# Optimization experiments

Measured on AMD Instinct MI355X. Metric: run time of the kernel, lower is better.

The kernel has to match this reference:

```python
import jax, jax.numpy as jnp
import numpy as np

N_AGENTS = 8
STATE_DIM = 256
EMBED_DIM = 32
BATCH = 65536


def setup_inputs() -> dict:
    key = jax.random.key(0)
    ks = jax.random.split(key, 12)
    s = 1.0 / np.sqrt(STATE_DIM)
    se = 1.0 / np.sqrt(EMBED_DIM)
    return {
        "agent_qs": jax.random.normal(ks[0], (BATCH, N_AGENTS), dtype=jnp.float32),
        "states": jax.random.normal(ks[1], (BATCH, STATE_DIM), dtype=jnp.float32),
        # hyper_w_1: Linear(state_dim, embed_dim * n_agents)
        "w1_W": jax.random.uniform(ks[2], (STATE_DIM, EMBED_DIM * N_AGENTS), jnp.float32, -s, s),
        "w1_b": jax.random.uniform(ks[3], (EMBED_DIM * N_AGENTS,), jnp.float32, -s, s),
        # hyper_w_final: Linear(state_dim, embed_dim)
        "wf_W": jax.random.uniform(ks[4], (STATE_DIM, EMBED_DIM), jnp.float32, -s, s),
        "wf_b": jax.random.uniform(ks[5], (EMBED_DIM,), jnp.float32, -s, s),
        # hyper_b_1: Linear(state_dim, embed_dim)
        "b1_W": jax.random.uniform(ks[6], (STATE_DIM, EMBED_DIM), jnp.float32, -s, s),
        "b1_b": jax.random.uniform(ks[7], (EMBED_DIM,), jnp.float32, -s, s),
        # V: Linear(state_dim, embed_dim) -> ReLU -> Linear(embed_dim, 1)
        "v1_W": jax.random.uniform(ks[8], (STATE_DIM, EMBED_DIM), jnp.float32, -s, s),
        "v1_b": jax.random.uniform(ks[9], (EMBED_DIM,), jnp.float32, -s, s),
        "v2_W": jax.random.uniform(ks[10], (EMBED_DIM, 1), jnp.float32, -se, se),
        "v2_b": jax.random.uniform(ks[11], (1,), jnp.float32, -se, se),
    }


def reference(agent_qs, states, w1_W, w1_b, wf_W, wf_b, b1_W, b1_b, v1_W, v1_b, v2_W, v2_b):
    B = agent_qs.shape[0]
    # hypernet weights (abs for monotonicity)
    w1 = jnp.abs(states @ w1_W + w1_b).reshape(B, N_AGENTS, EMBED_DIM)   # [B, A, E]
    w_final = jnp.abs(states @ wf_W + wf_b)                               # [B, E]
    b1 = states @ b1_W + b1_b                                             # [B, E]
    # hidden = elu(agent_qs^T w1 + b1): [B,1,A] @ [B,A,E] -> [B,E]
    hidden = jax.nn.elu(jnp.einsum("ba,bae->be", agent_qs, w1) + b1)
    # mixed = hidden @ w_final: [B,1,E] @ [B,E,1] -> [B,1]
    mixed = jnp.sum(hidden * w_final, axis=-1, keepdims=True)             # [B, 1]
    # state value V(s)
    state_value = jax.nn.relu(states @ v1_W + v1_b) @ v2_W + v2_b         # [B, 1]
    return mixed + state_value
```

## Files before the change

kernel.cpp:

```cpp
#include <hip/hip_runtime.h>
#include <math.h>


#define NTILES 22
#define KCHUNKS 8
#define CHUNK_I4 1408

typedef __attribute__((ext_vector_type(8))) short short8;
typedef __attribute__((ext_vector_type(4))) float float4v;

__device__ __forceinline__ unsigned short f2b(float f) {
    unsigned int u = __float_as_uint(f);
    u = u + 0x7fffu + ((u >> 16) & 1u);
    return (unsigned short)(u >> 16);
}

__device__ __forceinline__ void gl2lds16(const unsigned short* g, unsigned short* l) {
    __builtin_amdgcn_global_load_lds(
        (const __attribute__((address_space(1))) unsigned int*)g,
        (__attribute__((address_space(3))) unsigned int*)l,
        16, 0, 0);
}

__global__ void repack_b(const float* __restrict__ w1_W,
                         const float* __restrict__ wf_W,
                         const float* __restrict__ b1_W,
                         const float* __restrict__ v1_W,
                         unsigned short* __restrict__ brep) {
    int idx = blockIdx.x * 256 + threadIdx.x;
    int lane = idx & 63;
    int tt   = idx >> 6;
    int t    = tt % 22;
    int kc   = tt / 22;
    int kbase = kc * 32 + (lane >> 4) * 8;
    int n = t * 16 + (lane & 15);
    short8 frag;
#pragma unroll
    for (int j = 0; j < 8; ++j) {
        int k = kbase + j;
        float val;
        if (n < 256)      val = w1_W[k * 256 + n];
        else if (n < 288) val = wf_W[k * 32 + (n - 256)];
        else if (n < 320) val = b1_W[k * 32 + (n - 288)];
        else              val = v1_W[k * 32 + (n - 320)];
        frag[j] = (short)f2b(val);
    }
    *(short8*)(&brep[idx * 8]) = frag;
}

__global__ void __launch_bounds__(256, 2)
qmix_main(const float* __restrict__ agent_qs,
          const float* __restrict__ states,
          const unsigned short* __restrict__ brep,
          const float* __restrict__ w1_b,
          const float* __restrict__ wf_b,
          const float* __restrict__ b1_b,
          const float* __restrict__ v1_b,
          const float* __restrict__ v2_W,
          const float* __restrict__ v2_b,
          float* __restrict__ out) {
    __shared__ __align__(16) unsigned short wlds[2][NTILES * 64 * 8];

    const int tid  = threadIdx.x;
    const int wave = tid >> 6, lane = tid & 63;
    const int quad = lane >> 4, l16 = lane & 15;
    const int r0 = blockIdx.x * 128 + wave * 32 + l16;
    const float* srow0 = states + (size_t)r0 * 256;
    const float* srow1 = srow0 + 16 * 256;

    for (int s = wave; s < NTILES; s += 4)
        gl2lds16(brep + (size_t)(s * 64 + lane) * 8, wlds[0] + s * 512);

    float4v s0a = *(const float4v*)(srow0 + quad * 8);
    float4v s0b = *(const float4v*)(srow0 + quad * 8 + 4);
    float4v s1a = *(const float4v*)(srow1 + quad * 8);
    float4v s1b = *(const float4v*)(srow1 + quad * 8 + 4);

    float4v acc[2][NTILES];
#pragma unroll
    for (int g = 0; g < 2; ++g)
#pragma unroll
        for (int t = 0; t < NTILES; ++t)
#pragma unroll
            for (int q = 0; q < 4; ++q) acc[g][t][q] = 0.f;

    __syncthreads();

    int cur = 0;
    for (int kc = 0; kc < KCHUNKS; ++kc) {
        if (kc < KCHUNKS - 1) {
            const unsigned short* src = brep + (size_t)(kc + 1) * CHUNK_I4 * 8;
            unsigned short* dst = wlds[cur ^ 1];
            for (int s = wave; s < NTILES; s += 4)
                gl2lds16(src + (size_t)(s * 64 + lane) * 8, dst + s * 512);
        }
        short8 b0, b1;
#pragma unroll
        for (int j = 0; j < 4; ++j) {
            b0[j] = (short)f2b(s0a[j]); b0[4 + j] = (short)f2b(s0b[j]);
            b1[j] = (short)f2b(s1a[j]); b1[4 + j] = (short)f2b(s1b[j]);
        }
        if (kc < KCHUNKS - 1) {
            const float* p0 = srow0 + (kc + 1) * 32 + quad * 8;
            const float* p1 = srow1 + (kc + 1) * 32 + quad * 8;
            s0a = *(const float4v*)(p0);
            s0b = *(const float4v*)(p0 + 4);
            s1a = *(const float4v*)(p1);
            s1b = *(const float4v*)(p1 + 4);
        }
        const short8* wb = (const short8*)wlds[cur] + lane;
#pragma unroll
        for (int t = 0; t < NTILES; ++t) {
            short8 af = wb[t * 64];
            acc[0][t] = __builtin_amdgcn_mfma_f32_16x16x32_bf16(af, b0, acc[0][t], 0, 0, 0);
            acc[1][t] = __builtin_amdgcn_mfma_f32_16x16x32_bf16(af, b1, acc[1][t], 0, 0, 0);
        }
        cur ^= 1;
        __syncthreads();
    }

#pragma unroll
    for (int g = 0; g < 2; ++g) {
        const int row = r0 + g * 16;
        float4v q0 = *(const float4v*)(agent_qs + (size_t)row * 8);
        float4v q1 = *(const float4v*)(agent_qs + (size_t)row * 8 + 4);
        float qv[8] = {q0[0], q0[1], q0[2], q0[3], q1[0], q1[1], q1[2], q1[3]};

        float qacc[8], wfv[8], b1v[8], svp = 0.f;
#pragma unroll
        for (int s = 0; s < 8; ++s) qacc[s] = 0.f;

#pragma unroll
        for (int t = 0; t < NTILES; ++t) {
            const float* bptr =
                (t < 16) ? (w1_b + t * 16) :
                (t < 18) ? (wf_b + (t - 16) * 16) :
                (t < 20) ? (b1_b + (t - 18) * 16) : (v1_b + (t - 20) * 16);
            float4v bb = *(const float4v*)(bptr + quad * 4);
            float vb[4];
#pragma unroll
            for (int j = 0; j < 4; ++j) vb[j] = acc[g][t][j] + bb[j];

            if (t < 16) {
                float q = qv[t >> 1];
                int base = (t & 1) * 4;
#pragma unroll
                for (int j = 0; j < 4; ++j) qacc[base + j] += q * fabsf(vb[j]);
            } else if (t < 18) {
                int base = (t - 16) * 4;
#pragma unroll
                for (int j = 0; j < 4; ++j) wfv[base + j] = fabsf(vb[j]);
            } else if (t < 20) {
                int base = (t - 18) * 4;
#pragma unroll
                for (int j = 0; j < 4; ++j) b1v[base + j] = vb[j];
            } else {
                int ebase = (t - 20) * 16 + quad * 4;
#pragma unroll
                for (int j = 0; j < 4; ++j)
                    svp += fmaxf(vb[j], 0.f) * v2_W[ebase + j];
            }
        }

        float mix = 0.f;
#pragma unroll
        for (int s = 0; s < 8; ++s) {
            float h = qacc[s] + b1v[s];
            h = h > 0.f ? h : (__expf(h) - 1.f);
            mix += h * wfv[s];
        }
        float tot = mix + svp;
        tot += __shfl_xor(tot, 16);
        tot += __shfl_xor(tot, 32);
        if (quad == 0) out[row] = tot + v2_b[0];
    }
}

extern "C" void kernel_launch(void* const* d_in, const int* in_sizes, int n_in,
                              void* d_out, int out_size, void* d_ws, size_t ws_size,
                              hipStream_t stream) {
    const float* agent_qs = (const float*)d_in[0];
    const float* states   = (const float*)d_in[1];
    const float* w1_W = (const float*)d_in[2];
    const float* w1_b = (const float*)d_in[3];
    const float* wf_W = (const float*)d_in[4];
    const float* wf_b = (const float*)d_in[5];
    const float* b1_W = (const float*)d_in[6];
    const float* b1_b = (const float*)d_in[7];
    const float* v1_W = (const float*)d_in[8];
    const float* v1_b = (const float*)d_in[9];
    const float* v2_W = (const float*)d_in[10];
    const float* v2_b = (const float*)d_in[11];
    float* out = (float*)d_out;
    unsigned short* brep = (unsigned short*)d_ws;

    repack_b<<<44, 256, 0, stream>>>(w1_W, wf_W, b1_W, v1_W, brep);
    qmix_main<<<512, 256, 0, stream>>>(agent_qs, states, brep,
                                       w1_b, wf_b, b1_b, v1_b, v2_W, v2_b, out);
}
```

Before: 127.0 us.

## Keep w1 weights resident in LDS, stream small tiles from global, double block size

The repacked weights are reordered so all 16 w1 tiles across every K chunk (128 slots, 128 KB) are loaded into LDS once at kernel start. The remaining 6 tiles (wf, b1, v1) are read per chunk straight from global/L2 into registers. This removes the per-chunk double-buffered LDS refill and the __syncthreads in the K loop. Blocks grow to 512 threads covering 256 rows each, with half as many blocks. The 128 KB LDS footprint limits occupancy to at most one block per CU, even though launch bounds ask for two, and the direct global loads of the small tiles sit on the MFMA critical path.

```diff
diff --git a/kernel.cpp b/kernel.cpp
--- a/kernel.cpp
+++ b/kernel.cpp
@@ -4,7 +4,7 @@
 
 #define NTILES 22
 #define KCHUNKS 8
-#define CHUNK_I4 1408
+#define LDS_SLOTS 128
 
 typedef __attribute__((ext_vector_type(8))) short short8;
 typedef __attribute__((ext_vector_type(4))) float float4v;
@@ -29,9 +29,10 @@
                          unsigned short* __restrict__ brep) {
     int idx = blockIdx.x * 256 + threadIdx.x;
     int lane = idx & 63;
-    int tt   = idx >> 6;
-    int t    = tt % 22;
-    int kc   = tt / 22;
+    int slot = idx >> 6;
+    int t, kc;
+    if (slot < 128) { t = slot >> 3; kc = slot & 7; }
+    else            { int r = slot - 128; kc = r / 6; t = 16 + r % 6; }
     int kbase = kc * 32 + (lane >> 4) * 8;
     int n = t * 16 + (lane & 15);
     short8 frag;
@@ -48,7 +49,7 @@
     *(short8*)(&brep[idx * 8]) = frag;
 }
 
-__global__ void __launch_bounds__(256, 2)
+__global__ void __launch_bounds__(512, 2)
 qmix_main(const float* __restrict__ agent_qs,
           const float* __restrict__ states,
           const unsigned short* __restrict__ brep,
@@ -59,17 +60,17 @@
           const float* __restrict__ v2_W,
           const float* __restrict__ v2_b,
           float* __restrict__ out) {
-    __shared__ __align__(16) unsigned short wlds[2][NTILES * 64 * 8];
+    __shared__ __align__(16) unsigned short wlds[LDS_SLOTS * 64 * 8];
 
     const int tid  = threadIdx.x;
     const int wave = tid >> 6, lane = tid & 63;
     const int quad = lane >> 4, l16 = lane & 15;
-    const int r0 = blockIdx.x * 128 + wave * 32 + l16;
+    const int r0 = blockIdx.x * 256 + wave * 32 + l16;
     const float* srow0 = states + (size_t)r0 * 256;
     const float* srow1 = srow0 + 16 * 256;
 
-    for (int s = wave; s < NTILES; s += 4)
-        gl2lds16(brep + (size_t)(s * 64 + lane) * 8, wlds[0] + s * 512);
+    for (int s = wave; s < LDS_SLOTS; s += 8)
+        gl2lds16(brep + (size_t)(s * 64 + lane) * 8, wlds + s * 512);
 
     float4v s0a = *(const float4v*)(srow0 + quad * 8);
     float4v s0b = *(const float4v*)(srow0 + quad * 8 + 4);
@@ -86,14 +87,13 @@
 
     __syncthreads();
 
-    int cur = 0;
+    const short8* wl = (const short8*)wlds + lane;
+    const short8* ws = (const short8*)brep + LDS_SLOTS * 64 + lane;
+
     for (int kc = 0; kc < KCHUNKS; ++kc) {
-        if (kc < KCHUNKS - 1) {
-            const unsigned short* src = brep + (size_t)(kc + 1) * CHUNK_I4 * 8;
-            unsigned short* dst = wlds[cur ^ 1];
-            for (int s = wave; s < NTILES; s += 4)
-                gl2lds16(src + (size_t)(s * 64 + lane) * 8, dst + s * 512);
-        }
+        short8 sf[6];
+#pragma unroll
+        for (int u = 0; u < 6; ++u) sf[u] = ws[(kc * 6 + u) * 64];
         short8 b0, b1;
 #pragma unroll
         for (int j = 0; j < 4; ++j) {
@@ -108,15 +108,17 @@
             s1a = *(const float4v*)(p1);
             s1b = *(const float4v*)(p1 + 4);
         }
-        const short8* wb = (const short8*)wlds[cur] + lane;
-#pragma unroll
-        for (int t = 0; t < NTILES; ++t) {
-            short8 af = wb[t * 64];
+#pragma unroll
+        for (int t = 0; t < 16; ++t) {
+            short8 af = wl[(t * 8 + kc) * 64];
             acc[0][t] = __builtin_amdgcn_mfma_f32_16x16x32_bf16(af, b0, acc[0][t], 0, 0, 0);
             acc[1][t] = __builtin_amdgcn_mfma_f32_16x16x32_bf16(af, b1, acc[1][t], 0, 0, 0);
         }
-        cur ^= 1;
-        __syncthreads();
+#pragma unroll
+        for (int u = 0; u < 6; ++u) {
+            acc[0][16 + u] = __builtin_amdgcn_mfma_f32_16x16x32_bf16(sf[u], b0, acc[0][16 + u], 0, 0, 0);
+            acc[1][16 + u] = __builtin_amdgcn_mfma_f32_16x16x32_bf16(sf[u], b1, acc[1][16 + u], 0, 0, 0);
+        }
     }
 
 #pragma unroll
@@ -195,6 +197,6 @@
     unsigned short* brep = (unsigned short*)d_ws;
 
     repack_b<<<44, 256, 0, stream>>>(w1_W, wf_W, b1_W, v1_W, brep);
-    qmix_main<<<512, 256, 0, stream>>>(agent_qs, states, brep,
+    qmix_main<<<256, 512, 0, stream>>>(agent_qs, states, brep,
                                        w1_b, wf_b, b1_b, v1_b, v2_W, v2_b, out);
 }
```

After: 156.8 us. 1.23x slower.
